# Kernel optimization log

Hardware: AMD Instinct MI355X
Metric: run time of the kernel (lower is better)

Reference implementation:

```python
import jax, jax.numpy as jnp
import numpy as np

# ---- larq ste_sign: forward = sign (0 -> +1), backward = clipped straight-through ----
def _sign(x):
    return jnp.where(x >= 0, jnp.ones_like(x), -jnp.ones_like(x))

@jax.custom_vjp
def ste_sign(x):
    return _sign(x)

def _ste_fwd(x):
    return _sign(x), x

def _ste_bwd(x, g):
    return (g * (jnp.abs(x) <= 1.0).astype(g.dtype),)

ste_sign.defvjp(_ste_fwd, _ste_bwd)

BN_EPS = 1e-3  # keras BatchNormalization default epsilon

def conv2d(x, w, padding):
    # x: NHWC, w: HWIO
    return jax.lax.conv_general_dilated(
        x, w, window_strides=(1, 1), padding=padding,
        dimension_numbers=('NHWC', 'HWIO', 'NHWC'))

def maxpool2(x):
    return jax.lax.reduce_window(x, -jnp.inf, jax.lax.max,
                                 (1, 2, 2, 1), (1, 2, 2, 1), 'VALID')

def batchnorm(x, mean, var, beta):
    # BatchNormalization(scale=False): gamma fixed at 1
    return (x - mean) * jax.lax.rsqrt(var + BN_EPS) + beta


def setup_inputs() -> dict:
    key = jax.random.key(0)
    ks = jax.random.split(key, 20)
    d = {}
    d['x'] = jax.random.normal(ks[0], (64, 128, 128, 3), dtype=jnp.float32)
    d['w1'] = jax.random.normal(ks[1], (3, 3, 3, 32), dtype=jnp.float32)
    d['m1'] = jax.random.normal(ks[2], (32,), dtype=jnp.float32)
    d['v1'] = jax.random.uniform(ks[3], (32,), dtype=jnp.float32)
    d['b1'] = jax.random.normal(ks[4], (32,), dtype=jnp.float32)
    d['w2'] = jax.random.normal(ks[5], (3, 3, 32, 64), dtype=jnp.float32)
    d['m2'] = jax.random.normal(ks[6], (64,), dtype=jnp.float32)
    d['v2'] = jax.random.uniform(ks[7], (64,), dtype=jnp.float32)
    d['b2'] = jax.random.normal(ks[8], (64,), dtype=jnp.float32)
    d['w3'] = jax.random.normal(ks[9], (3, 3, 64, 128), dtype=jnp.float32)
    d['m3'] = jax.random.normal(ks[10], (128,), dtype=jnp.float32)
    d['v3'] = jax.random.uniform(ks[11], (128,), dtype=jnp.float32)
    d['b3'] = jax.random.normal(ks[12], (128,), dtype=jnp.float32)
    d['w4'] = jax.random.normal(ks[13], (3, 3, 128, 256), dtype=jnp.float32)
    d['m4'] = jax.random.normal(ks[14], (256,), dtype=jnp.float32)
    d['v4'] = jax.random.uniform(ks[15], (256,), dtype=jnp.float32)
    d['b4'] = jax.random.normal(ks[16], (256,), dtype=jnp.float32)
    return d


def reference(x, w1, m1, v1, b1, w2, m2, v2, b2, w3, m3, v3, b3, w4, m4, v4, b4):
    # Stem: QuantConv2D(32,3x3,valid) with kernel quantized only (no input quantizer)
    y = conv2d(x, ste_sign(w1), 'VALID')          # [B,126,126,32]
    y = batchnorm(maxpool2(y), m1, v1, b1)        # [B,63,63,32]
    # Three binarized blocks: ste_sign(input) conv ste_sign(kernel), same padding
    for w, m, v, b in ((w2, m2, v2, b2), (w3, m3, v3, b3), (w4, m4, v4, b4)):
        y = conv2d(ste_sign(y), ste_sign(w), 'SAME')
        y = batchnorm(maxpool2(y), m, v, b)       # halves spatial dims
    return y                                      # [B,7,7,256]
```

## Files before the change

### kernel.cpp

```cpp
#include <hip/hip_runtime.h>
#include <stdint.h>

#define BN_EPS 1e-3f

template <int CIN, int COUT>
__device__ inline void packw(const float* __restrict__ w, uint32_t* __restrict__ wp, int idx) {
    const int CINW = CIN / 32;
    int co = idx % COUT;
    int t2 = idx / COUT;
    int wi = t2 % CINW;
    int tap = t2 / CINW;
    uint32_t word = 0;
#pragma unroll
    for (int bb = 0; bb < 32; bb++) {
        float val = w[((tap * CIN) + wi * 32 + bb) * COUT + co];
        word |= (uint32_t)(val < 0.f) << bb;
    }
    wp[idx] = word;
}

__global__ void pack_all(const float* __restrict__ w1, const float* __restrict__ w2,
                         const float* __restrict__ w3, const float* __restrict__ w4,
                         float* __restrict__ w1s, uint32_t* __restrict__ w2p,
                         uint32_t* __restrict__ w3p, uint32_t* __restrict__ w4p) {
    int idx = blockIdx.x * 256 + threadIdx.x;
    if (idx < 864) {
        w1s[idx] = (w1[idx] < 0.f) ? -1.f : 1.f;
        return;
    }
    idx -= 864;
    if (idx < 576) { packw<32, 64>(w2, w2p, idx); return; }
    idx -= 576;
    if (idx < 2304) { packw<64, 128>(w3, w3p, idx); return; }
    idx -= 2304;
    if (idx < 9216) { packw<128, 256>(w4, w4p, idx); return; }
}

__global__ __launch_bounds__(256, 4) void conv1_k(const float* __restrict__ x,
                                                  const float* __restrict__ w1s,
                                                  const float* __restrict__ m1,
                                                  const float* __restrict__ v1,
                                                  const float* __restrict__ b1,
                                                  uint32_t* __restrict__ y1p) {
    __shared__ __align__(16) float xt[34 * 104];

    int tile = blockIdx.x;
    int tx = tile & 3;
    int ty = (tile >> 2) & 3;
    int n  = tile >> 4;
    int ph0 = ty * 16, pw0 = tx * 16;
    int r0 = 2 * ph0;
    int cf0 = pw0 * 6;

    for (int i = threadIdx.x; i < 34 * 102; i += 256) {
        int r = i / 102, c = i % 102;
        int gr = r0 + r, gcf = cf0 + c;
        float vv = 0.f;
        if (gr < 128 && gcf < 384)
            vv = x[(size_t)(n * 128 + gr) * 384 + gcf];
        xt[r * 104 + c] = vv;
    }
    __syncthreads();

    int wave = threadIdx.x >> 6, lane = threadIdx.x & 63;
    int px = lane & 15, py = (wave << 2) + (lane >> 4);
    int ph = ph0 + py, pw = pw0 + px;

    float win[48];
#pragma unroll
    for (int r = 0; r < 4; r++) {
        const float2* bp = (const float2*)&xt[(2 * py + r) * 104 + 6 * px];
#pragma unroll
        for (int q = 0; q < 6; q++) {
            float2 f2 = bp[q];
            win[r * 12 + 2 * q]     = f2.x;
            win[r * 12 + 2 * q + 1] = f2.y;
        }
    }

    uint32_t word = 0;
#pragma unroll 1
    for (int g = 0; g < 4; g++) {
        float acc[8][4];
#pragma unroll
        for (int j = 0; j < 8; j++)
#pragma unroll
            for (int p = 0; p < 4; p++) acc[j][p] = 0.f;

        const float* sgc = w1s + g * 8;
#pragma unroll
        for (int kh = 0; kh < 3; kh++)
#pragma unroll
            for (int kw = 0; kw < 3; kw++)
#pragma unroll
                for (int ci = 0; ci < 3; ci++) {
                    int tap = (kh * 3 + kw) * 3 + ci;
                    float x00 = win[kh * 12 + kw * 3 + ci];
                    float x01 = win[kh * 12 + (kw + 1) * 3 + ci];
                    float x10 = win[(kh + 1) * 12 + kw * 3 + ci];
                    float x11 = win[(kh + 1) * 12 + (kw + 1) * 3 + ci];
                    float4 s0 = *(const float4*)(sgc + tap * 32);
                    float4 s1 = *(const float4*)(sgc + tap * 32 + 4);
                    float sv[8] = {s0.x, s0.y, s0.z, s0.w, s1.x, s1.y, s1.z, s1.w};
#pragma unroll
                    for (int j = 0; j < 8; j++) {
                        acc[j][0] += x00 * sv[j];
                        acc[j][1] += x01 * sv[j];
                        acc[j][2] += x10 * sv[j];
                        acc[j][3] += x11 * sv[j];
                    }
                }
#pragma unroll
        for (int j = 0; j < 8; j++) {
            float mx = fmaxf(fmaxf(acc[j][0], acc[j][1]), fmaxf(acc[j][2], acc[j][3]));
            int ch = g * 8 + j;
            float y = (mx - m1[ch]) * rsqrtf(v1[ch] + BN_EPS) + b1[ch];
            word |= (uint32_t)(y < 0.f) << ch;
        }
    }

    if (ph < 63 && pw < 63)
        y1p[(n * 63 + ph) * 63 + pw] = word;
}

__global__ __launch_bounds__(256) void bconv2(const uint32_t* __restrict__ y1p,
                                              const uint32_t* __restrict__ w2p,
                                              const float* __restrict__ m,
                                              const float* __restrict__ v,
                                              const float* __restrict__ b,
                                              uint2* __restrict__ y2p) {
    __shared__ uint32_t tile[4 * 64];

    int blk = blockIdx.x;
    int ph = blk % 31;
    int n  = blk / 31;
    int lane = threadIdx.x & 63;
    int wave = threadIdx.x >> 6;

    int row0 = 2 * ph - 1;
    for (int i = threadIdx.x; i < 4 * 63; i += 256) {
        int r = i / 63, c = i % 63;
        int rr = min(max(row0 + r, 0), 62);
        tile[r * 64 + c] = y1p[(n * 63 + rr) * 63 + c];
    }
    __syncthreads();

    uint32_t wq[9];
#pragma unroll
    for (int tap = 0; tap < 9; tap++) wq[tap] = w2p[tap * 64 + lane];
    float mm = m[lane];
    float rs = rsqrtf(v[lane] + BN_EPS);
    float bb = b[lane];

#pragma unroll 1
    for (int pw = wave; pw < 31; pw += 4) {
        int best = -1000000;
#pragma unroll 1
        for (int q = 0; q < 4; q++) {
            int dy = q >> 1, dx = q & 1;
            int oh = 2 * ph + dy, ow = 2 * pw + dx;
            int acc = 0, K = 0;
#pragma unroll
            for (int kh = 0; kh < 3; kh++) {
                int ih = oh - 1 + kh;
                bool rok = (ih >= 0) && (ih < 63);
#pragma unroll
                for (int kw = 0; kw < 3; kw++) {
                    int iw = ow - 1 + kw;
                    bool ok = rok && (iw >= 0) && (iw < 63);
                    uint32_t wv = tile[(dy + kh) * 64 + min(max(iw, 0), 62)];
                    acc += ok ? __popc(wv ^ wq[kh * 3 + kw]) : 0;
                    K += ok ? 32 : 0;
                }
            }
            best = max(best, K - 2 * acc);
        }
        float y = ((float)best - mm) * rs + bb;
        unsigned long long bal = __ballot(y < 0.f);
        if (lane == 0)
            y2p[(n * 31 + ph) * 31 + pw] = make_uint2((uint32_t)bal, (uint32_t)(bal >> 32));
    }
}

__global__ __launch_bounds__(256) void bconv3(const uint2* __restrict__ y2p,
                                              const uint32_t* __restrict__ w3p,
                                              const float* __restrict__ m,
                                              const float* __restrict__ v,
                                              const float* __restrict__ b,
                                              uint32_t* __restrict__ y3p) {
    __shared__ uint2 tile[4 * 32];

    int blk = blockIdx.x;
    int ph = blk % 15;
    int n  = blk / 15;
    int lane = threadIdx.x & 63;
    int wave = threadIdx.x >> 6;
    int half = wave & 1;
    int co = half * 64 + lane;

    int row0 = 2 * ph - 1;
    for (int i = threadIdx.x; i < 4 * 31; i += 256) {
        int r = i / 31, c = i % 31;
        int rr = min(max(row0 + r, 0), 30);
        tile[r * 32 + c] = y2p[(n * 31 + rr) * 31 + c];
    }
    __syncthreads();

    uint32_t wq0[9], wq1[9];
#pragma unroll
    for (int tap = 0; tap < 9; tap++) {
        wq0[tap] = w3p[(tap * 2 + 0) * 128 + co];
        wq1[tap] = w3p[(tap * 2 + 1) * 128 + co];
    }
    float mm = m[co];
    float rs = rsqrtf(v[co] + BN_EPS);
    float bb = b[co];

#pragma unroll 1
    for (int pw = (wave >> 1); pw < 15; pw += 2) {
        int best = -1000000;
#pragma unroll 1
        for (int q = 0; q < 4; q++) {
            int dy = q >> 1, dx = q & 1;
            int oh = 2 * ph + dy, ow = 2 * pw + dx;
            int acc = 0, K = 0;
#pragma unroll
            for (int kh = 0; kh < 3; kh++) {
                int ih = oh - 1 + kh;
                bool rok = (ih >= 0) && (ih < 31);
#pragma unroll
                for (int kw = 0; kw < 3; kw++) {
                    int iw = ow - 1 + kw;
                    bool ok = rok && (iw >= 0) && (iw < 31);
                    uint2 iv = tile[(dy + kh) * 32 + min(max(iw, 0), 30)];
                    int tap = kh * 3 + kw;
                    acc += ok ? (__popc(iv.x ^ wq0[tap]) + __popc(iv.y ^ wq1[tap])) : 0;
                    K += ok ? 64 : 0;
                }
            }
            best = max(best, K - 2 * acc);
        }
        float y = ((float)best - mm) * rs + bb;
        unsigned long long bal = __ballot(y < 0.f);
        uint32_t val = (lane & 1) ? (uint32_t)(bal >> 32) : (uint32_t)bal;
        if (lane < 2) {
            int pixel = (n * 15 + ph) * 15 + pw;
            y3p[pixel * 4 + half * 2 + lane] = val;
        }
    }
}

__global__ __launch_bounds__(256) void bconv4(const uint4* __restrict__ y3p,
                                              const uint32_t* __restrict__ w4p,
                                              const float* __restrict__ m,
                                              const float* __restrict__ v,
                                              const float* __restrict__ b,
                                              float* __restrict__ out) {
    __shared__ __align__(16) uint32_t tile[64];

    int pixel = blockIdx.x;
    int lane = threadIdx.x & 63;
    int co = (threadIdx.x >> 6) * 64 + lane;
    int pw = pixel % 7;
    int t = pixel / 7;
    int ph = t % 7;
    int n = t / 7;

    if (threadIdx.x < 64) {
        int tt = threadIdx.x;
        int r = tt >> 4, e = (tt >> 2) & 3, w = tt & 3;
        int gr = 2 * ph - 1 + r, gc = 2 * pw - 1 + e;
        uint32_t val = 0;
        if (gr >= 0 && gr < 15 && gc >= 0 && gc < 15)
            val = ((const uint32_t*)y3p)[(((size_t)(n * 15 + gr) * 15 + gc) << 2) + w];
        tile[tt] = val;
    }
    __syncthreads();

    const uint4* tp = (const uint4*)tile;

    uint4 wq[9];
#pragma unroll
    for (int tap = 0; tap < 9; tap++) {
        wq[tap].x = w4p[(tap * 4 + 0) * 256 + co];
        wq[tap].y = w4p[(tap * 4 + 1) * 256 + co];
        wq[tap].z = w4p[(tap * 4 + 2) * 256 + co];
        wq[tap].w = w4p[(tap * 4 + 3) * 256 + co];
    }

    int best = -1000000;
#pragma unroll 1
    for (int q = 0; q < 4; q++) {
        int dy = q >> 1, dx = q & 1;
        int oh = 2 * ph + dy, ow = 2 * pw + dx;
        int acc = 0, K = 0;
#pragma unroll
        for (int kh = 0; kh < 3; kh++) {
            int ih = oh - 1 + kh;
            bool rok = (ih >= 0) && (ih < 15);
#pragma unroll
            for (int kw = 0; kw < 3; kw++) {
                int iw = ow - 1 + kw;
                bool ok = rok && (iw >= 0) && (iw < 15);
                uint4 iv = tp[(dy + kh) * 4 + (dx + kw)];
                int tap = kh * 3 + kw;
                int pc = __popc(iv.x ^ wq[tap].x) + __popc(iv.y ^ wq[tap].y)
                       + __popc(iv.z ^ wq[tap].z) + __popc(iv.w ^ wq[tap].w);
                acc += ok ? pc : 0;
                K += ok ? 128 : 0;
            }
        }
        best = max(best, K - 2 * acc);
    }
    float y = ((float)best - m[co]) * rsqrtf(v[co] + BN_EPS) + b[co];
    out[pixel * 256 + co] = y;
}

extern "C" void kernel_launch(void* const* d_in, const int* in_sizes, int n_in,
                              void* d_out, int out_size, void* d_ws, size_t ws_size,
                              hipStream_t stream) {
    const float* x  = (const float*)d_in[0];
    const float* w1 = (const float*)d_in[1];
    const float* m1 = (const float*)d_in[2];
    const float* v1 = (const float*)d_in[3];
    const float* b1 = (const float*)d_in[4];
    const float* w2 = (const float*)d_in[5];
    const float* m2 = (const float*)d_in[6];
    const float* v2 = (const float*)d_in[7];
    const float* b2 = (const float*)d_in[8];
    const float* w3 = (const float*)d_in[9];
    const float* m3 = (const float*)d_in[10];
    const float* v3 = (const float*)d_in[11];
    const float* b3 = (const float*)d_in[12];
    const float* w4 = (const float*)d_in[13];
    const float* m4 = (const float*)d_in[14];
    const float* v4 = (const float*)d_in[15];
    const float* b4 = (const float*)d_in[16];
    float* out = (float*)d_out;

    char* ws = (char*)d_ws;
    size_t off = 0;
    auto take = [&](size_t bytes) -> char* {
        char* p = ws + off;
        off += (bytes + 255) & ~(size_t)255;
        return p;
    };
    uint32_t* y1p = (uint32_t*)take((size_t)64 * 63 * 63 * 4);
    uint2*    y2p = (uint2*)take((size_t)64 * 31 * 31 * 8);
    uint32_t* y3p = (uint32_t*)take((size_t)64 * 15 * 15 * 16);
    float*    w1s = (float*)take(864 * 4);
    uint32_t* w2p = (uint32_t*)take(576 * 4);
    uint32_t* w3p = (uint32_t*)take(2304 * 4);
    uint32_t* w4p = (uint32_t*)take(9216 * 4);

    pack_all<<<(864 + 576 + 2304 + 9216 + 255) / 256, 256, 0, stream>>>(
        w1, w2, w3, w4, w1s, w2p, w3p, w4p);

    conv1_k<<<64 * 16, 256, 0, stream>>>(x, w1s, m1, v1, b1, y1p);

    bconv2<<<64 * 31, 256, 0, stream>>>(y1p, w2p, m2, v2, b2, y2p);

    bconv3<<<64 * 15, 256, 0, stream>>>(y2p, w3p, m3, v3, b3, y3p);

    bconv4<<<64 * 7 * 7, 256, 0, stream>>>((const uint4*)y3p, w4p, m4, v4, b4, out);
}
```

Baseline: 195.4 us.

## Fuse all four conv stages into one kernel with row-band halo recompute

Replaces the four per-layer kernels with one kernel in which each block handles a quarter of an image's output rows. Every intermediate activation stays in shared memory, and the overlapping halo rows are recomputed instead of written to and read back from global memory. This removes the intermediate global traffic and three launches. The cost is only 256 blocks of 512 threads, which is low occupancy on a large GPU, plus duplicated stem conv work in the halos (30 stem rows computed per 16 needed).

Result: slower. 360.2 us (+84.3%).

```diff
diff --git a/kernel.cpp b/kernel.cpp
--- a/kernel.cpp
+++ b/kernel.cpp
@@ -36,284 +36,265 @@
     if (idx < 9216) { packw<128, 256>(w4, w4p, idx); return; }
 }
 
-__global__ __launch_bounds__(256, 4) void conv1_k(const float* __restrict__ x,
-                                                  const float* __restrict__ w1s,
-                                                  const float* __restrict__ m1,
-                                                  const float* __restrict__ v1,
-                                                  const float* __restrict__ b1,
-                                                  uint32_t* __restrict__ y1p) {
-    __shared__ __align__(16) float xt[34 * 104];
-
-    int tile = blockIdx.x;
-    int tx = tile & 3;
-    int ty = (tile >> 2) & 3;
-    int n  = tile >> 4;
-    int ph0 = ty * 16, pw0 = tx * 16;
-    int r0 = 2 * ph0;
-    int cf0 = pw0 * 6;
-
-    for (int i = threadIdx.x; i < 34 * 102; i += 256) {
-        int r = i / 102, c = i % 102;
-        int gr = r0 + r, gcf = cf0 + c;
-        float vv = 0.f;
-        if (gr < 128 && gcf < 384)
-            vv = x[(size_t)(n * 128 + gr) * 384 + gcf];
-        xt[r * 104 + c] = vv;
+__global__ __launch_bounds__(512, 2) void mono_k(
+        const float* __restrict__ x,  const float* __restrict__ w1,
+        const float* __restrict__ m1, const float* __restrict__ v1, const float* __restrict__ b1,
+        const uint32_t* __restrict__ w2p,
+        const float* __restrict__ m2, const float* __restrict__ v2, const float* __restrict__ b2,
+        const uint32_t* __restrict__ w3p,
+        const float* __restrict__ m3, const float* __restrict__ v3, const float* __restrict__ b3,
+        const uint32_t* __restrict__ w4p,
+        const float* __restrict__ m4, const float* __restrict__ v4, const float* __restrict__ b4,
+        float* __restrict__ out) {
+    __shared__ __align__(16) float    xt[34 * 200];
+    __shared__ __align__(16) float    wsgn[864];
+    __shared__ uint32_t               y1s[30 * 64];
+    __shared__ uint2                  y2s[14 * 32];
+    __shared__ __align__(16) uint32_t y3s[6 * 15 * 4];
+
+    const int blk = blockIdx.x;
+    const int q = blk & 3;
+    const int n = blk >> 2;
+    const int tid = threadIdx.x;
+    const int wave = tid >> 6, lane = tid & 63;
+
+    const int y1lo = max(0, 16 * q - 7),  y1hi = min(62, 16 * q + 22);
+    const int y2lo = max(0, 8 * q - 3),   y2hi = min(30, 8 * q + 10);
+    const int y3lo = max(0, 4 * q - 1),   y3hi = min(14, 4 * q + 4);
+    const int olo  = 2 * q,               ohi  = min(6, 2 * q + 1);
+    const int ny1 = y1hi - y1lo + 1;
+    const int ny2 = y2hi - y2lo + 1;
+    const int ny3 = y3hi - y3lo + 1;
+    const int no  = ohi - olo + 1;
+
+    for (int i = tid; i < 864; i += 512)
+        wsgn[i] = (w1[i] < 0.f) ? -1.f : 1.f;
+
+    {
+        int py = (wave & 3) * 4 + (lane >> 4);
+        int px = (wave >> 2) * 16 + (lane & 15);
+#pragma unroll 1
+        for (int rc = 0; rc < 2; rc++) {
+            int rowbase = y1lo + rc * 16;
+#pragma unroll 1
+            for (int cc = 0; cc < 2; cc++) {
+                int colbase = cc * 32;
+                int r0 = 2 * rowbase;
+                int cf0 = colbase * 6;
+                __syncthreads();
+                for (int i = tid; i < 34 * 198; i += 512) {
+                    int r = i / 198, c = i % 198;
+                    int gr = r0 + r, gcf = cf0 + c;
+                    float vv = 0.f;
+                    if (gr < 128 && gcf < 384)
+                        vv = x[(size_t)(n * 128 + gr) * 384 + gcf];
+                    xt[r * 200 + c] = vv;
+                }
+                __syncthreads();
+
+                float win[48];
+#pragma unroll
+                for (int r = 0; r < 4; r++) {
+                    const float2* bp = (const float2*)&xt[(2 * py + r) * 200 + 6 * px];
+#pragma unroll
+                    for (int qq = 0; qq < 6; qq++) {
+                        float2 f2 = bp[qq];
+                        win[r * 12 + 2 * qq]     = f2.x;
+                        win[r * 12 + 2 * qq + 1] = f2.y;
+                    }
+                }
+
+                uint32_t word = 0;
+#pragma unroll 1
+                for (int g = 0; g < 4; g++) {
+                    float acc[8][4];
+#pragma unroll
+                    for (int j = 0; j < 8; j++)
+#pragma unroll
+                        for (int p = 0; p < 4; p++) acc[j][p] = 0.f;
+
+#pragma unroll
+                    for (int kh = 0; kh < 3; kh++)
+#pragma unroll
+                        for (int kw = 0; kw < 3; kw++)
+#pragma unroll
+                            for (int ci = 0; ci < 3; ci++) {
+                                int tap = (kh * 3 + kw) * 3 + ci;
+                                float x00 = win[kh * 12 + kw * 3 + ci];
+                                float x01 = win[kh * 12 + (kw + 1) * 3 + ci];
+                                float x10 = win[(kh + 1) * 12 + kw * 3 + ci];
+                                float x11 = win[(kh + 1) * 12 + (kw + 1) * 3 + ci];
+                                float4 s0 = *(const float4*)(&wsgn[tap * 32 + g * 8]);
+                                float4 s1 = *(const float4*)(&wsgn[tap * 32 + g * 8 + 4]);
+                                float sv[8] = {s0.x, s0.y, s0.z, s0.w, s1.x, s1.y, s1.z, s1.w};
+#pragma unroll
+                                for (int j = 0; j < 8; j++) {
+                                    acc[j][0] += x00 * sv[j];
+                                    acc[j][1] += x01 * sv[j];
+                                    acc[j][2] += x10 * sv[j];
+                                    acc[j][3] += x11 * sv[j];
+                                }
+                            }
+#pragma unroll
+                    for (int j = 0; j < 8; j++) {
+                        float mx = fmaxf(fmaxf(acc[j][0], acc[j][1]), fmaxf(acc[j][2], acc[j][3]));
+                        int ch = g * 8 + j;
+                        float y = (mx - m1[ch]) * rsqrtf(v1[ch] + BN_EPS) + b1[ch];
+                        word |= (uint32_t)(y < 0.f) << ch;
+                    }
+                }
+
+                int srow = rc * 16 + py;
+                int pw = colbase + px;
+                if (srow < ny1 && pw < 63)
+                    y1s[srow * 64 + pw] = word;
+            }
+        }
     }
     __syncthreads();
 
-    int wave = threadIdx.x >> 6, lane = threadIdx.x & 63;
-    int px = lane & 15, py = (wave << 2) + (lane >> 4);
-    int ph = ph0 + py, pw = pw0 + px;
-
-    float win[48];
-#pragma unroll
-    for (int r = 0; r < 4; r++) {
-        const float2* bp = (const float2*)&xt[(2 * py + r) * 104 + 6 * px];
-#pragma unroll
-        for (int q = 0; q < 6; q++) {
-            float2 f2 = bp[q];
-            win[r * 12 + 2 * q]     = f2.x;
-            win[r * 12 + 2 * q + 1] = f2.y;
-        }
-    }
-
-    uint32_t word = 0;
-#pragma unroll 1
-    for (int g = 0; g < 4; g++) {
-        float acc[8][4];
-#pragma unroll
-        for (int j = 0; j < 8; j++)
-#pragma unroll
-            for (int p = 0; p < 4; p++) acc[j][p] = 0.f;
-
-        const float* sgc = w1s + g * 8;
-#pragma unroll
-        for (int kh = 0; kh < 3; kh++)
-#pragma unroll
-            for (int kw = 0; kw < 3; kw++)
-#pragma unroll
-                for (int ci = 0; ci < 3; ci++) {
-                    int tap = (kh * 3 + kw) * 3 + ci;
-                    float x00 = win[kh * 12 + kw * 3 + ci];
-                    float x01 = win[kh * 12 + (kw + 1) * 3 + ci];
-                    float x10 = win[(kh + 1) * 12 + kw * 3 + ci];
-                    float x11 = win[(kh + 1) * 12 + (kw + 1) * 3 + ci];
-                    float4 s0 = *(const float4*)(sgc + tap * 32);
-                    float4 s1 = *(const float4*)(sgc + tap * 32 + 4);
-                    float sv[8] = {s0.x, s0.y, s0.z, s0.w, s1.x, s1.y, s1.z, s1.w};
-#pragma unroll
-                    for (int j = 0; j < 8; j++) {
-                        acc[j][0] += x00 * sv[j];
-                        acc[j][1] += x01 * sv[j];
-                        acc[j][2] += x10 * sv[j];
-                        acc[j][3] += x11 * sv[j];
-                    }
-                }
-#pragma unroll
-        for (int j = 0; j < 8; j++) {
-            float mx = fmaxf(fmaxf(acc[j][0], acc[j][1]), fmaxf(acc[j][2], acc[j][3]));
-            int ch = g * 8 + j;
-            float y = (mx - m1[ch]) * rsqrtf(v1[ch] + BN_EPS) + b1[ch];
-            word |= (uint32_t)(y < 0.f) << ch;
-        }
-    }
-
-    if (ph < 63 && pw < 63)
-        y1p[(n * 63 + ph) * 63 + pw] = word;
-}
-
-__global__ __launch_bounds__(256) void bconv2(const uint32_t* __restrict__ y1p,
-                                              const uint32_t* __restrict__ w2p,
-                                              const float* __restrict__ m,
-                                              const float* __restrict__ v,
-                                              const float* __restrict__ b,
-                                              uint2* __restrict__ y2p) {
-    __shared__ uint32_t tile[4 * 64];
-
-    int blk = blockIdx.x;
-    int ph = blk % 31;
-    int n  = blk / 31;
-    int lane = threadIdx.x & 63;
-    int wave = threadIdx.x >> 6;
-
-    int row0 = 2 * ph - 1;
-    for (int i = threadIdx.x; i < 4 * 63; i += 256) {
-        int r = i / 63, c = i % 63;
-        int rr = min(max(row0 + r, 0), 62);
-        tile[r * 64 + c] = y1p[(n * 63 + rr) * 63 + c];
+    {
+        uint32_t wq[9];
+#pragma unroll
+        for (int tap = 0; tap < 9; tap++) wq[tap] = w2p[tap * 64 + lane];
+        float mm = m2[lane];
+        float rs = rsqrtf(v2[lane] + BN_EPS);
+        float bb = b2[lane];
+
+        int ntask = ny2 * 31;
+#pragma unroll 1
+        for (int idx = wave; idx < ntask; idx += 8) {
+            int r2 = y2lo + idx / 31;
+            int pw = idx % 31;
+            int best = -1000000;
+#pragma unroll 1
+            for (int qq = 0; qq < 4; qq++) {
+                int dy = qq >> 1, dx = qq & 1;
+                int oh = 2 * r2 + dy, ow = 2 * pw + dx;
+                int acc = 0, K = 0;
+#pragma unroll
+                for (int kh = 0; kh < 3; kh++) {
+                    int ih = oh - 1 + kh;
+                    bool rok = (ih >= 0) && (ih < 63);
+                    int rowS = min(max(ih, y1lo), y1hi) - y1lo;
+#pragma unroll
+                    for (int kw = 0; kw < 3; kw++) {
+                        int iw = ow - 1 + kw;
+                        bool ok = rok && (iw >= 0) && (iw < 63);
+                        uint32_t wv = y1s[rowS * 64 + min(max(iw, 0), 62)];
+                        acc += ok ? __popc(wv ^ wq[kh * 3 + kw]) : 0;
+                        K += ok ? 32 : 0;
+                    }
+                }
+                best = max(best, K - 2 * acc);
+            }
+            float y = ((float)best - mm) * rs + bb;
+            unsigned long long bal = __ballot(y < 0.f);
+            if (lane == 0)
+                y2s[(r2 - y2lo) * 32 + pw] = make_uint2((uint32_t)bal, (uint32_t)(bal >> 32));
+        }
     }
     __syncthreads();
 
-    uint32_t wq[9];
-#pragma unroll
-    for (int tap = 0; tap < 9; tap++) wq[tap] = w2p[tap * 64 + lane];
-    float mm = m[lane];
-    float rs = rsqrtf(v[lane] + BN_EPS);
-    float bb = b[lane];
-
-#pragma unroll 1
-    for (int pw = wave; pw < 31; pw += 4) {
-        int best = -1000000;
-#pragma unroll 1
-        for (int q = 0; q < 4; q++) {
-            int dy = q >> 1, dx = q & 1;
-            int oh = 2 * ph + dy, ow = 2 * pw + dx;
-            int acc = 0, K = 0;
-#pragma unroll
-            for (int kh = 0; kh < 3; kh++) {
-                int ih = oh - 1 + kh;
-                bool rok = (ih >= 0) && (ih < 63);
-#pragma unroll
-                for (int kw = 0; kw < 3; kw++) {
-                    int iw = ow - 1 + kw;
-                    bool ok = rok && (iw >= 0) && (iw < 63);
-                    uint32_t wv = tile[(dy + kh) * 64 + min(max(iw, 0), 62)];
-                    acc += ok ? __popc(wv ^ wq[kh * 3 + kw]) : 0;
-                    K += ok ? 32 : 0;
-                }
+    {
+        int half = wave & 1;
+        int co = half * 64 + lane;
+        uint32_t wq0[9], wq1[9];
+#pragma unroll
+        for (int tap = 0; tap < 9; tap++) {
+            wq0[tap] = w3p[(tap * 2 + 0) * 128 + co];
+            wq1[tap] = w3p[(tap * 2 + 1) * 128 + co];
+        }
+        float mm = m3[co];
+        float rs = rsqrtf(v3[co] + BN_EPS);
+        float bb = b3[co];
+
+        int ntask = ny3 * 15;
+#pragma unroll 1
+        for (int t2 = (wave >> 1); t2 < ntask; t2 += 4) {
+            int r3 = y3lo + t2 / 15;
+            int pw = t2 % 15;
+            int best = -1000000;
+#pragma unroll 1
+            for (int qq = 0; qq < 4; qq++) {
+                int dy = qq >> 1, dx = qq & 1;
+                int oh = 2 * r3 + dy, ow = 2 * pw + dx;
+                int acc = 0, K = 0;
+#pragma unroll
+                for (int kh = 0; kh < 3; kh++) {
+                    int ih = oh - 1 + kh;
+                    bool rok = (ih >= 0) && (ih < 31);
+                    int rowS = min(max(ih, y2lo), y2hi) - y2lo;
+#pragma unroll
+                    for (int kw = 0; kw < 3; kw++) {
+                        int iw = ow - 1 + kw;
+                        bool ok = rok && (iw >= 0) && (iw < 31);
+                        uint2 iv = y2s[rowS * 32 + min(max(iw, 0), 30)];
+                        int tap = kh * 3 + kw;
+                        acc += ok ? (__popc(iv.x ^ wq0[tap]) + __popc(iv.y ^ wq1[tap])) : 0;
+                        K += ok ? 64 : 0;
+                    }
+                }
+                best = max(best, K - 2 * acc);
             }
-            best = max(best, K - 2 * acc);
-        }
-        float y = ((float)best - mm) * rs + bb;
-        unsigned long long bal = __ballot(y < 0.f);
-        if (lane == 0)
-            y2p[(n * 31 + ph) * 31 + pw] = make_uint2((uint32_t)bal, (uint32_t)(bal >> 32));
-    }
-}
-
-__global__ __launch_bounds__(256) void bconv3(const uint2* __restrict__ y2p,
-                                              const uint32_t* __restrict__ w3p,
-                                              const float* __restrict__ m,
-                                              const float* __restrict__ v,
-                                              const float* __restrict__ b,
-                                              uint32_t* __restrict__ y3p) {
-    __shared__ uint2 tile[4 * 32];
-
-    int blk = blockIdx.x;
-    int ph = blk % 15;
-    int n  = blk / 15;
-    int lane = threadIdx.x & 63;
-    int wave = threadIdx.x >> 6;
-    int half = wave & 1;
-    int co = half * 64 + lane;
-
-    int row0 = 2 * ph - 1;
-    for (int i = threadIdx.x; i < 4 * 31; i += 256) {
-        int r = i / 31, c = i % 31;
-        int rr = min(max(row0 + r, 0), 30);
-        tile[r * 32 + c] = y2p[(n * 31 + rr) * 31 + c];
+            float y = ((float)best - mm) * rs + bb;
+            unsigned long long bal = __ballot(y < 0.f);
+            uint32_t val = (lane & 1) ? (uint32_t)(bal >> 32) : (uint32_t)bal;
+            if (lane < 2)
+                y3s[((r3 - y3lo) * 15 + pw) * 4 + half * 2 + lane] = val;
+        }
     }
     __syncthreads();
 
-    uint32_t wq0[9], wq1[9];
-#pragma unroll
-    for (int tap = 0; tap < 9; tap++) {
-        wq0[tap] = w3p[(tap * 2 + 0) * 128 + co];
-        wq1[tap] = w3p[(tap * 2 + 1) * 128 + co];
-    }
-    float mm = m[co];
-    float rs = rsqrtf(v[co] + BN_EPS);
-    float bb = b[co];
-
-#pragma unroll 1
-    for (int pw = (wave >> 1); pw < 15; pw += 2) {
-        int best = -1000000;
-#pragma unroll 1
-        for (int q = 0; q < 4; q++) {
-            int dy = q >> 1, dx = q & 1;
-            int oh = 2 * ph + dy, ow = 2 * pw + dx;
-            int acc = 0, K = 0;
-#pragma unroll
-            for (int kh = 0; kh < 3; kh++) {
-                int ih = oh - 1 + kh;
-                bool rok = (ih >= 0) && (ih < 31);
-#pragma unroll
-                for (int kw = 0; kw < 3; kw++) {
-                    int iw = ow - 1 + kw;
-                    bool ok = rok && (iw >= 0) && (iw < 31);
-                    uint2 iv = tile[(dy + kh) * 32 + min(max(iw, 0), 30)];
-                    int tap = kh * 3 + kw;
-                    acc += ok ? (__popc(iv.x ^ wq0[tap]) + __popc(iv.y ^ wq1[tap])) : 0;
-                    K += ok ? 64 : 0;
-                }
+    {
+        int grp = wave & 3;
+        int co = grp * 64 + lane;
+        uint4 wq[9];
+#pragma unroll
+        for (int tap = 0; tap < 9; tap++) {
+            wq[tap].x = w4p[(tap * 4 + 0) * 256 + co];
+            wq[tap].y = w4p[(tap * 4 + 1) * 256 + co];
+            wq[tap].z = w4p[(tap * 4 + 2) * 256 + co];
+            wq[tap].w = w4p[(tap * 4 + 3) * 256 + co];
+        }
+        float mm = m4[co];
+        float rs = rsqrtf(v4[co] + BN_EPS);
+        float bb = b4[co];
+
+        int ntask = no * 7;
+#pragma unroll 1
+        for (int u = (wave >> 2); u < ntask; u += 2) {
+            int o = olo + u / 7;
+            int pw = u % 7;
+            int best = -1000000;
+#pragma unroll 1
+            for (int qq = 0; qq < 4; qq++) {
+                int dy = qq >> 1, dx = qq & 1;
+                int oh = 2 * o + dy, ow = 2 * pw + dx;
+                int acc = 0, K = 0;
+#pragma unroll
+                for (int kh = 0; kh < 3; kh++) {
+                    int ih = oh - 1 + kh;
+                    bool rok = (ih >= 0) && (ih < 15);
+                    int rowS = min(max(ih, y3lo), y3hi) - y3lo;
+#pragma unroll
+                    for (int kw = 0; kw < 3; kw++) {
+                        int iw = ow - 1 + kw;
+                        bool ok = rok && (iw >= 0) && (iw < 15);
+                        const uint4 iv = *(const uint4*)&y3s[(rowS * 15 + min(max(iw, 0), 14)) * 4];
+                        int tap = kh * 3 + kw;
+                        int pc = __popc(iv.x ^ wq[tap].x) + __popc(iv.y ^ wq[tap].y)
+                               + __popc(iv.z ^ wq[tap].z) + __popc(iv.w ^ wq[tap].w);
+                        acc += ok ? pc : 0;
+                        K += ok ? 128 : 0;
+                    }
+                }
+                best = max(best, K - 2 * acc);
             }
-            best = max(best, K - 2 * acc);
-        }
-        float y = ((float)best - mm) * rs + bb;
-        unsigned long long bal = __ballot(y < 0.f);
-        uint32_t val = (lane & 1) ? (uint32_t)(bal >> 32) : (uint32_t)bal;
-        if (lane < 2) {
-            int pixel = (n * 15 + ph) * 15 + pw;
-            y3p[pixel * 4 + half * 2 + lane] = val;
-        }
-    }
-}
-
-__global__ __launch_bounds__(256) void bconv4(const uint4* __restrict__ y3p,
-                                              const uint32_t* __restrict__ w4p,
-                                              const float* __restrict__ m,
-                                              const float* __restrict__ v,
-                                              const float* __restrict__ b,
-                                              float* __restrict__ out) {
-    __shared__ __align__(16) uint32_t tile[64];
-
-    int pixel = blockIdx.x;
-    int lane = threadIdx.x & 63;
-    int co = (threadIdx.x >> 6) * 64 + lane;
-    int pw = pixel % 7;
-    int t = pixel / 7;
-    int ph = t % 7;
-    int n = t / 7;
-
-    if (threadIdx.x < 64) {
-        int tt = threadIdx.x;
-        int r = tt >> 4, e = (tt >> 2) & 3, w = tt & 3;
-        int gr = 2 * ph - 1 + r, gc = 2 * pw - 1 + e;
-        uint32_t val = 0;
-        if (gr >= 0 && gr < 15 && gc >= 0 && gc < 15)
-            val = ((const uint32_t*)y3p)[(((size_t)(n * 15 + gr) * 15 + gc) << 2) + w];
-        tile[tt] = val;
-    }
-    __syncthreads();
-
-    const uint4* tp = (const uint4*)tile;
-
-    uint4 wq[9];
-#pragma unroll
-    for (int tap = 0; tap < 9; tap++) {
-        wq[tap].x = w4p[(tap * 4 + 0) * 256 + co];
-        wq[tap].y = w4p[(tap * 4 + 1) * 256 + co];
-        wq[tap].z = w4p[(tap * 4 + 2) * 256 + co];
-        wq[tap].w = w4p[(tap * 4 + 3) * 256 + co];
-    }
-
-    int best = -1000000;
-#pragma unroll 1
-    for (int q = 0; q < 4; q++) {
-        int dy = q >> 1, dx = q & 1;
-        int oh = 2 * ph + dy, ow = 2 * pw + dx;
-        int acc = 0, K = 0;
-#pragma unroll
-        for (int kh = 0; kh < 3; kh++) {
-            int ih = oh - 1 + kh;
-            bool rok = (ih >= 0) && (ih < 15);
-#pragma unroll
-            for (int kw = 0; kw < 3; kw++) {
-                int iw = ow - 1 + kw;
-                bool ok = rok && (iw >= 0) && (iw < 15);
-                uint4 iv = tp[(dy + kh) * 4 + (dx + kw)];
-                int tap = kh * 3 + kw;
-                int pc = __popc(iv.x ^ wq[tap].x) + __popc(iv.y ^ wq[tap].y)
-                       + __popc(iv.z ^ wq[tap].z) + __popc(iv.w ^ wq[tap].w);
-                acc += ok ? pc : 0;
-                K += ok ? 128 : 0;
-            }
-        }
-        best = max(best, K - 2 * acc);
-    }
-    float y = ((float)best - m[co]) * rsqrtf(v[co] + BN_EPS) + b[co];
-    out[pixel * 256 + co] = y;
+            float y = ((float)best - mm) * rs + bb;
+            out[((size_t)(n * 7 + o) * 7 + pw) * 256 + co] = y;
+        }
+    }
 }
 
 extern "C" void kernel_launch(void* const* d_in, const int* in_sizes, int n_in,
@@ -345,9 +326,6 @@
         off += (bytes + 255) & ~(size_t)255;
         return p;
     };
-    uint32_t* y1p = (uint32_t*)take((size_t)64 * 63 * 63 * 4);
-    uint2*    y2p = (uint2*)take((size_t)64 * 31 * 31 * 8);
-    uint32_t* y3p = (uint32_t*)take((size_t)64 * 15 * 15 * 16);
     float*    w1s = (float*)take(864 * 4);
     uint32_t* w2p = (uint32_t*)take(576 * 4);
     uint32_t* w3p = (uint32_t*)take(2304 * 4);
@@ -356,11 +334,10 @@
     pack_all<<<(864 + 576 + 2304 + 9216 + 255) / 256, 256, 0, stream>>>(
         w1, w2, w3, w4, w1s, w2p, w3p, w4p);
 
-    conv1_k<<<64 * 16, 256, 0, stream>>>(x, w1s, m1, v1, b1, y1p);
-
-    bconv2<<<64 * 31, 256, 0, stream>>>(y1p, w2p, m2, v2, b2, y2p);
-
-    bconv3<<<64 * 15, 256, 0, stream>>>(y2p, w3p, m3, v3, b3, y3p);
-
-    bconv4<<<64 * 7 * 7, 256, 0, stream>>>((const uint4*)y3p, w4p, m4, v4, b4, out);
+    mono_k<<<64 * 4, 512, 0, stream>>>(
+        x, w1, m1, v1, b1,
+        w2p, m2, v2, b2,
+        w3p, m3, v3, b3,
+        w4p, m4, v4, b4,
+        out);
 }
```
